# Kernel optimization log

Measured on AMD Instinct MI355X. Metric: run time of the kernel, lower is better.

Reference implementation:

```python
import jax, jax.numpy as jnp
import numpy as np

NUM_GRAPHS = 256
NEG_SLOPE = 0.2


def gat_layer(x, src, dst, W, a_src, a_dst, bias, concat):
    # x: [N, Fin], W: [Fin, H*C], a_src/a_dst: [H, C], bias: [H*C] or [C]
    N = x.shape[0]
    H, C = a_src.shape
    xl = (x @ W).reshape(N, H, C)                      # per-head projections
    e_src = jnp.sum(xl * a_src, axis=-1)               # [N, H]
    e_dst = jnp.sum(xl * a_dst, axis=-1)               # [N, H]
    e = jax.nn.leaky_relu(e_src[src] + e_dst[dst], NEG_SLOPE)  # [E, H]
    # edge softmax over variable-size neighbor sets (grouped by dst)
    m = jax.ops.segment_max(e, dst, num_segments=N)    # [N, H]
    m = jnp.where(jnp.isfinite(m), m, 0.0)
    ee = jnp.exp(e - m[dst])
    s = jax.ops.segment_sum(ee, dst, num_segments=N)   # [N, H]
    alpha = ee / (s[dst] + 1e-16)                      # [E, H]
    msg = alpha[:, :, None] * xl[src]                  # [E, H, C]
    out = jax.ops.segment_sum(msg, dst, num_segments=N)  # [N, H, C]
    out = out.reshape(N, H * C) if concat else out.mean(axis=1)
    return out + bias


def setup_inputs() -> dict:
    key = jax.random.key(0)
    ks = jax.random.split(key, 12)
    N, E, Fin, H, C, Fout = 100000, 1600000, 128, 8, 16, 64
    x = jax.random.normal(ks[0], (N, Fin), dtype=jnp.float32)
    edge_index = jax.random.randint(ks[1], (2, E), 0, N, dtype=jnp.int32)
    batch = jnp.sort(jax.random.randint(ks[2], (N,), 0, NUM_GRAPHS, dtype=jnp.int32))
    sc = 0.1
    W1 = jax.random.normal(ks[3], (Fin, H * C), dtype=jnp.float32) * sc
    att_src1 = jax.random.normal(ks[4], (H, C), dtype=jnp.float32) * sc
    att_dst1 = jax.random.normal(ks[5], (H, C), dtype=jnp.float32) * sc
    bias1 = jnp.zeros((H * C,), dtype=jnp.float32)
    W2 = jax.random.normal(ks[6], (H * C, Fout), dtype=jnp.float32) * sc
    att_src2 = jax.random.normal(ks[7], (1, Fout), dtype=jnp.float32) * sc
    att_dst2 = jax.random.normal(ks[8], (1, Fout), dtype=jnp.float32) * sc
    bias2 = jnp.zeros((Fout,), dtype=jnp.float32)
    return {"x": x, "W1": W1, "att_src1": att_src1, "att_dst1": att_dst1,
            "bias1": bias1, "W2": W2, "att_src2": att_src2, "att_dst2": att_dst2,
            "bias2": bias2, "edge_index": edge_index, "batch": batch}


def reference(x, W1, att_src1, att_dst1, bias1, W2, att_src2, att_dst2, bias2,
              edge_index, batch):
    N = x.shape[0]
    loop = jnp.arange(N, dtype=edge_index.dtype)
    src = jnp.concatenate([edge_index[0], loop])  # add self-loops (PyG default)
    dst = jnp.concatenate([edge_index[1], loop])
    # dropout is identity in eval mode
    h = gat_layer(x, src, dst, W1, att_src1, att_dst1, bias1, concat=True)
    h = jax.nn.elu(h)
    h = gat_layer(h, src, dst, W2, att_src2, att_dst2, bias2, concat=False)
    # global mean pooling over graphs
    sums = jax.ops.segment_sum(h, batch, num_segments=NUM_GRAPHS)
    cnts = jax.ops.segment_sum(jnp.ones((N,), h.dtype), batch, num_segments=NUM_GRAPHS)
    return sums / jnp.maximum(cnts, 1.0)[:, None]
```

## Files before the change

### kernel.cpp

```cpp
#include <hip/hip_runtime.h>
#include <hip/hip_fp16.h>


#define LRELU_SLOPE 0.2f
#define NBLKB 512
#define NBUCK 256

__device__ __forceinline__ float lrelu(float x) { return x > 0.f ? x : LRELU_SLOPE * x; }

typedef _Float16 f16x8 __attribute__((ext_vector_type(8)));
typedef float f32x4 __attribute__((ext_vector_type(4)));

__global__ __launch_bounds__(256) void convWT(const float* __restrict__ W,
    __half* __restrict__ Wt, int K, int M) {
  const int i = blockIdx.x * 256 + threadIdx.x;
  if (i < K * M) {
    const int k = i / M, m = i % M;
    Wt[m * K + k] = __float2half(W[i]);
  }
}

template<typename TX, int M_>
__global__ __launch_bounds__(256) void gemm_mfma(const TX* __restrict__ X,
    const __half* __restrict__ Wt, __half* __restrict__ Y, int N) {
  constexpr int K = 128;
  constexpr int BM = 64;
  constexpr int LP = K + 8;
  __shared__ _Float16 Xl[BM * LP];
  const int tid = threadIdx.x;
  const int row0 = blockIdx.x * BM;

  if constexpr (sizeof(TX) == 4) {
    for (int i = tid; i < BM * (K / 4); i += 256) {
      const int r = i / (K / 4), c4 = (i % (K / 4)) * 4;
      int gr = row0 + r; if (gr >= N) gr = N - 1;
      const float4 v = *(const float4*)((const float*)X + (size_t)gr * K + c4);
      _Float16* d = &Xl[r * LP + c4];
      d[0] = (_Float16)v.x; d[1] = (_Float16)v.y;
      d[2] = (_Float16)v.z; d[3] = (_Float16)v.w;
    }
  } else {
    for (int i = tid; i < BM * (K / 8); i += 256) {
      const int r = i / (K / 8), c8 = (i % (K / 8)) * 8;
      int gr = row0 + r; if (gr >= N) gr = N - 1;
      const f16x8 v = *(const f16x8*)((const _Float16*)X + (size_t)gr * K + c8);
      *(f16x8*)&Xl[r * LP + c8] = v;
    }
  }
  __syncthreads();

  const int w = tid >> 6, l = tid & 63;
  const int lrow = l & 15, lk = (l >> 4) * 8;
  constexpr int NT = M_ / 16;
  f32x4 acc[NT];
#pragma unroll
  for (int n = 0; n < NT; ++n) acc[n] = (f32x4){0.f, 0.f, 0.f, 0.f};

#pragma unroll
  for (int kk = 0; kk < K; kk += 32) {
    const f16x8 a = *(const f16x8*)&Xl[(w * 16 + lrow) * LP + kk + lk];
#pragma unroll
    for (int n = 0; n < NT; ++n) {
      const f16x8 b = *(const f16x8*)((const _Float16*)Wt +
                        (size_t)(n * 16 + lrow) * K + kk + lk);
      acc[n] = __builtin_amdgcn_mfma_f32_16x16x32_f16(a, b, acc[n], 0, 0, 0);
    }
  }
  const int orow = row0 + w * 16 + (l >> 4) * 4;
#pragma unroll
  for (int n = 0; n < NT; ++n) {
#pragma unroll
    for (int j = 0; j < 4; ++j) {
      const int gr = orow + j;
      if (gr < N) Y[(size_t)gr * M_ + n * 16 + lrow] = __float2half(acc[n][j]);
    }
  }
}

__global__ __launch_bounds__(256) void att_h8(const __half* __restrict__ xl,
    const float* __restrict__ as, const float* __restrict__ ad,
    float* __restrict__ es, float* __restrict__ ed, int N) {
  const int n = blockIdx.x * 2 + (threadIdx.x >> 7);
  const int c = threadIdx.x & 127;
  if (n >= N) return;
  const float v = __half2float(xl[(size_t)n * 128 + c]);
  float ps = v * as[c];
  float pd = v * ad[c];
#pragma unroll
  for (int o = 8; o >= 1; o >>= 1) {
    ps += __shfl_xor(ps, o, 16);
    pd += __shfl_xor(pd, o, 16);
  }
  if ((c & 15) == 0) {
    es[n * 8 + (c >> 4)] = ps;
    ed[n * 8 + (c >> 4)] = pd;
  }
}

__global__ __launch_bounds__(256) void att_h1(const __half* __restrict__ xl2,
    const float* __restrict__ as, const float* __restrict__ ad,
    float* __restrict__ es, float* __restrict__ ed, int N) {
  const int n = blockIdx.x * 4 + (threadIdx.x >> 6);
  const int c = threadIdx.x & 63;
  if (n >= N) return;
  const float v = __half2float(xl2[(size_t)n * 64 + c]);
  float ps = v * as[c];
  float pd = v * ad[c];
#pragma unroll
  for (int o = 32; o >= 1; o >>= 1) {
    ps += __shfl_xor(ps, o, 64);
    pd += __shfl_xor(pd, o, 64);
  }
  if (c == 0) { es[n] = ps; ed[n] = pd; }
}

__global__ __launch_bounds__(256) void bucket_hist(const int* __restrict__ ei, int E,
    int* __restrict__ bh) {
  __shared__ int hist[NBUCK];
  const int t = threadIdx.x;
  hist[t] = 0;
  __syncthreads();
  const int chunk = (E + NBLKB - 1) / NBLKB;
  const int s0 = blockIdx.x * chunk;
  const int s1 = min(E, s0 + chunk);
  for (int e = s0 + t; e < s1; e += 256) atomicAdd(&hist[ei[E + e] >> 9], 1);
  __syncthreads();
  bh[t * NBLKB + blockIdx.x] = hist[t];
}

__global__ __launch_bounds__(256) void scanA(int* __restrict__ a, int* __restrict__ ctot, int N) {
  __shared__ int sm[256];
  const int base = blockIdx.x * 1024;
  const int t = threadIdx.x;
  int v[4], s = 0;
#pragma unroll
  for (int i = 0; i < 4; ++i) {
    const int idx = base + t * 4 + i;
    v[i] = (idx < N) ? a[idx] : 0;
    s += v[i];
  }
  sm[t] = s;
  __syncthreads();
  for (int o = 1; o < 256; o <<= 1) {
    const int x = (t >= o) ? sm[t - o] : 0;
    __syncthreads();
    sm[t] += x;
    __syncthreads();
  }
  if (t == 255) ctot[blockIdx.x] = sm[255];
  int run = sm[t] - s;
#pragma unroll
  for (int i = 0; i < 4; ++i) {
    const int idx = base + t * 4 + i;
    if (idx < N) a[idx] = run;
    run += v[i];
  }
}

__global__ __launch_bounds__(128) void scanB(int* __restrict__ ctot, int n) {
  __shared__ int sm[128];
  const int t = threadIdx.x;
  const int v = (t < n) ? ctot[t] : 0;
  sm[t] = v;
  __syncthreads();
  for (int o = 1; o < 128; o <<= 1) {
    const int x = (t >= o) ? sm[t - o] : 0;
    __syncthreads();
    sm[t] += x;
    __syncthreads();
  }
  if (t < n) ctot[t] = sm[t] - v;
}

__global__ __launch_bounds__(256) void scanC(int* __restrict__ a, const int* __restrict__ ctot, int N) {
  const int i = blockIdx.x * 256 + threadIdx.x;
  if (i < N) a[i] += ctot[i >> 10];
}

__global__ __launch_bounds__(256) void bucket_scatter(const int* __restrict__ ei, int E,
    const int* __restrict__ bh, int2* __restrict__ eb) {
  __shared__ int offs[NBUCK];
  const int t = threadIdx.x;
  offs[t] = bh[t * NBLKB + blockIdx.x];
  __syncthreads();
  const int chunk = (E + NBLKB - 1) / NBLKB;
  const int s0 = blockIdx.x * chunk;
  const int s1 = min(E, s0 + chunk);
  for (int e = s0 + t; e < s1; e += 256) {
    const int s = ei[e], d = ei[E + e];
    const int pos = atomicAdd(&offs[d >> 9], 1);
    eb[pos] = make_int2(s, d);
  }
}

__global__ __launch_bounds__(256) void csr_bucket(const int2* __restrict__ eb,
    const int* __restrict__ bh, int E, int N,
    int* __restrict__ rowptr, int* __restrict__ csr) {
  __shared__ int deg[512];
  __shared__ int sm[256];
  const int t = threadIdx.x;
  const int bucket = blockIdx.x;
  const int bstart = bh[bucket * NBLKB];
  const int bend = (bucket + 1 < NBUCK) ? bh[(bucket + 1) * NBLKB] : E;
  const int n0 = bucket << 9;
  deg[t] = 0; deg[t + 256] = 0;
  __syncthreads();
  for (int j = bstart + t; j < bend; j += 256) atomicAdd(&deg[eb[j].y - n0], 1);
  __syncthreads();
  const int v0 = deg[2 * t], v1 = deg[2 * t + 1];
  const int s = v0 + v1;
  sm[t] = s;
  __syncthreads();
  for (int o = 1; o < 256; o <<= 1) {
    const int x = (t >= o) ? sm[t - o] : 0;
    __syncthreads();
    sm[t] += x;
    __syncthreads();
  }
  const int base = sm[t] - s;
  if (n0 + 2 * t < N)     rowptr[n0 + 2 * t]     = bstart + base + v0;
  if (n0 + 2 * t + 1 < N) rowptr[n0 + 2 * t + 1] = bstart + base + v0 + v1;
  deg[2 * t] = base;
  deg[2 * t + 1] = base + v0;
  __syncthreads();
  for (int j = bstart + t; j < bend; j += 256) {
    const int2 e = eb[j];
    const int pos = bstart + atomicAdd(&deg[e.y - n0], 1);
    csr[pos] = e.x;
  }
}

__global__ __launch_bounds__(256) void gather_h8(const __half* __restrict__ xl,
    const float* __restrict__ es, const float* __restrict__ ed,
    const int* __restrict__ rowptr, const int* __restrict__ csr,
    const float* __restrict__ bias, __half* __restrict__ hout, int N) {
  const int wave = threadIdx.x >> 6, lane = threadIdx.x & 63;
  const int n = blockIdx.x * 4 + wave;
  if (n >= N) return;
  const int sub = lane >> 5;
  const int sl  = lane & 31;
  const int c0  = sl * 4;
  const int h   = sl >> 2;
  const float edv = ed[n * 8 + h];
  const int start = (n == 0) ? 0 : rowptr[n - 1];
  const int end   = rowptr[n];
  union U8 { uint2 u; __half2 h2[2]; };

  float4 acc = make_float4(0.f, 0.f, 0.f, 0.f);
  float ssum = 0.f;
  if (sub == 0) {
    const float ee = __expf(lrelu(es[n * 8 + h] + edv));
    U8 r; r.u = *(const uint2*)&xl[(size_t)n * 128 + c0];
    const float2 f0 = __half22float2(r.h2[0]), f1 = __half22float2(r.h2[1]);
    acc.x = ee * f0.x; acc.y = ee * f0.y; acc.z = ee * f1.x; acc.w = ee * f1.y;
    ssum = ee;
  }
  int j = start + sub;
  for (; j + 6 < end; j += 8) {
    int s0 = csr[j], s1 = csr[j + 2], s2 = csr[j + 4], s3 = csr[j + 6];
    float ev[4]; U8 r[4];
    ev[0] = es[s0 * 8 + h]; r[0].u = *(const uint2*)&xl[(size_t)s0 * 128 + c0];
    ev[1] = es[s1 * 8 + h]; r[1].u = *(const uint2*)&xl[(size_t)s1 * 128 + c0];
    ev[2] = es[s2 * 8 + h]; r[2].u = *(const uint2*)&xl[(size_t)s2 * 128 + c0];
    ev[3] = es[s3 * 8 + h]; r[3].u = *(const uint2*)&xl[(size_t)s3 * 128 + c0];
#pragma unroll
    for (int k = 0; k < 4; ++k) {
      const float ee = __expf(lrelu(ev[k] + edv));
      const float2 f0 = __half22float2(r[k].h2[0]), f1 = __half22float2(r[k].h2[1]);
      acc.x += ee * f0.x; acc.y += ee * f0.y;
      acc.z += ee * f1.x; acc.w += ee * f1.y;
      ssum += ee;
    }
  }
  for (; j < end; j += 2) {
    const int src = csr[j];
    const float ee = __expf(lrelu(es[src * 8 + h] + edv));
    U8 r; r.u = *(const uint2*)&xl[(size_t)src * 128 + c0];
    const float2 f0 = __half22float2(r.h2[0]), f1 = __half22float2(r.h2[1]);
    acc.x += ee * f0.x; acc.y += ee * f0.y;
    acc.z += ee * f1.x; acc.w += ee * f1.y;
    ssum += ee;
  }
  acc.x += __shfl_xor(acc.x, 32); acc.y += __shfl_xor(acc.y, 32);
  acc.z += __shfl_xor(acc.z, 32); acc.w += __shfl_xor(acc.w, 32);
  ssum  += __shfl_xor(ssum, 32);
  if (sub == 0) {
    const float inv = 1.f / (ssum + 1e-16f);
    const float4 b4 = *(const float4*)&bias[c0];
    float v0 = acc.x * inv + b4.x, v1 = acc.y * inv + b4.y;
    float v2 = acc.z * inv + b4.z, v3 = acc.w * inv + b4.w;
    v0 = v0 > 0.f ? v0 : __expf(v0) - 1.f;
    v1 = v1 > 0.f ? v1 : __expf(v1) - 1.f;
    v2 = v2 > 0.f ? v2 : __expf(v2) - 1.f;
    v3 = v3 > 0.f ? v3 : __expf(v3) - 1.f;
    U8 o; o.h2[0] = __floats2half2_rn(v0, v1); o.h2[1] = __floats2half2_rn(v2, v3);
    *(uint2*)&hout[(size_t)n * 128 + c0] = o.u;
  }
}

__global__ __launch_bounds__(256) void gather_h1(const __half* __restrict__ xl2,
    const float* __restrict__ es, const float* __restrict__ ed,
    const int* __restrict__ rowptr, const int* __restrict__ csr,
    const float* __restrict__ bias, float* __restrict__ vout, int N) {
  const int wave = threadIdx.x >> 6, lane = threadIdx.x & 63;
  const int n = blockIdx.x * 4 + wave;
  if (n >= N) return;
  const int sub = lane >> 4;
  const int sl  = lane & 15;
  const int c0  = sl * 4;
  const float edv = ed[n];
  const int start = (n == 0) ? 0 : rowptr[n - 1];
  const int end   = rowptr[n];
  union U8 { uint2 u; __half2 h2[2]; };

  float4 acc = make_float4(0.f, 0.f, 0.f, 0.f);
  float ssum = 0.f;
  if (sub == 0) {
    const float ee = __expf(lrelu(es[n] + edv));
    U8 r; r.u = *(const uint2*)&xl2[(size_t)n * 64 + c0];
    const float2 f0 = __half22float2(r.h2[0]), f1 = __half22float2(r.h2[1]);
    acc.x = ee * f0.x; acc.y = ee * f0.y; acc.z = ee * f1.x; acc.w = ee * f1.y;
    ssum = ee;
  }
  int j = start + sub;
  for (; j + 4 < end; j += 8) {
    const int s0 = csr[j], s1 = csr[j + 4];
    const float e0 = es[s0], e1 = es[s1];
    U8 r0, r1;
    r0.u = *(const uint2*)&xl2[(size_t)s0 * 64 + c0];
    r1.u = *(const uint2*)&xl2[(size_t)s1 * 64 + c0];
    {
      const float ee = __expf(lrelu(e0 + edv));
      const float2 f0 = __half22float2(r0.h2[0]), f1 = __half22float2(r0.h2[1]);
      acc.x += ee * f0.x; acc.y += ee * f0.y;
      acc.z += ee * f1.x; acc.w += ee * f1.y; ssum += ee;
    }
    {
      const float ee = __expf(lrelu(e1 + edv));
      const float2 f0 = __half22float2(r1.h2[0]), f1 = __half22float2(r1.h2[1]);
      acc.x += ee * f0.x; acc.y += ee * f0.y;
      acc.z += ee * f1.x; acc.w += ee * f1.y; ssum += ee;
    }
  }
  for (; j < end; j += 4) {
    const int src = csr[j];
    const float ee = __expf(lrelu(es[src] + edv));
    U8 r; r.u = *(const uint2*)&xl2[(size_t)src * 64 + c0];
    const float2 f0 = __half22float2(r.h2[0]), f1 = __half22float2(r.h2[1]);
    acc.x += ee * f0.x; acc.y += ee * f0.y;
    acc.z += ee * f1.x; acc.w += ee * f1.y; ssum += ee;
  }
#pragma unroll
  for (int o = 16; o <= 32; o <<= 1) {
    acc.x += __shfl_xor(acc.x, o); acc.y += __shfl_xor(acc.y, o);
    acc.z += __shfl_xor(acc.z, o); acc.w += __shfl_xor(acc.w, o);
    ssum  += __shfl_xor(ssum, o);
  }
  if (sub == 0) {
    const float inv = 1.f / (ssum + 1e-16f);
    const float4 b4 = *(const float4*)&bias[c0];
    float4 o;
    o.x = acc.x * inv + b4.x; o.y = acc.y * inv + b4.y;
    o.z = acc.z * inv + b4.z; o.w = acc.w * inv + b4.w;
    *(float4*)&vout[(size_t)n * 64 + c0] = o;
  }
}

__global__ __launch_bounds__(256) void pool_seg(const float* __restrict__ v,
    const int* __restrict__ batch, float* __restrict__ out, int N) {
  const int g = blockIdx.x;
  const int t = threadIdx.x;
  int lo = 0, hi = N;
  while (lo < hi) { const int m = (lo + hi) >> 1; if (batch[m] < g) lo = m + 1; else hi = m; }
  const int start = lo;
  hi = N;
  while (lo < hi) { const int m = (lo + hi) >> 1; if (batch[m] <= g) lo = m + 1; else hi = m; }
  const int end = lo;

  const int c = t & 63, rg = t >> 6;
  float s = 0.f;
  for (int r = start + rg; r < end; r += 4) s += v[(size_t)r * 64 + c];
  __shared__ float sm[256];
  sm[t] = s;
  __syncthreads();
  if (t < 64) {
    const float tot = sm[t] + sm[t + 64] + sm[t + 128] + sm[t + 192];
    out[g * 64 + t] = tot / fmaxf((float)(end - start), 1.f);
  }
}

extern "C" void kernel_launch(void* const* d_in, const int* in_sizes, int n_in,
                              void* d_out, int out_size, void* d_ws, size_t ws_size,
                              hipStream_t stream) {
  const float* x   = (const float*)d_in[0];
  const float* W1  = (const float*)d_in[1];
  const float* as1 = (const float*)d_in[2];
  const float* ad1 = (const float*)d_in[3];
  const float* b1  = (const float*)d_in[4];
  const float* W2  = (const float*)d_in[5];
  const float* as2 = (const float*)d_in[6];
  const float* ad2 = (const float*)d_in[7];
  const float* b2  = (const float*)d_in[8];
  const int* ei    = (const int*)d_in[9];
  const int* batch = (const int*)d_in[10];
  float* out = (float*)d_out;
  const int N = in_sizes[10];
  const int E = in_sizes[9] / 2;
  const int G = out_size / 64;
  const int BH = NBUCK * NBLKB;

  char* ws = (char*)d_ws;
  __half* xl  = (__half*)ws;
  __half* h   = (__half*)(ws + (size_t)N * 256);
  __half* xl2 = xl;
  float* vbuf = (float*)(ws + (size_t)N * 256);
  float* es1  = (float*)(ws + (size_t)N * 512);
  float* ed1  = es1 + (size_t)N * 8;
  float* es2  = es1;
  float* ed2  = es1 + N;
  int* rowptr = (int*)(ed1 + (size_t)N * 8);
  int* csr    = rowptr + N;
  int2* eb    = (int2*)((((uintptr_t)(csr + E)) + 7) & ~(uintptr_t)7);
  int* bh     = (int*)(eb + E);
  int* ctot   = bh + BH;
  __half* Wt1 = (__half*)((((uintptr_t)(ctot + 128)) + 31) & ~(uintptr_t)31);
  __half* Wt2 = Wt1 + 128 * 128;

  convWT<<<(128 * 128 + 255) / 256, 256, 0, stream>>>(W1, Wt1, 128, 128);
  convWT<<<(128 * 64 + 255) / 256, 256, 0, stream>>>(W2, Wt2, 128, 64);

  bucket_hist<<<NBLKB, 256, 0, stream>>>(ei, E, bh);
  scanA<<<BH / 1024, 256, 0, stream>>>(bh, ctot, BH);
  scanB<<<1, 128, 0, stream>>>(ctot, BH / 1024);
  scanC<<<BH / 256, 256, 0, stream>>>(bh, ctot, BH);
  bucket_scatter<<<NBLKB, 256, 0, stream>>>(ei, E, bh, eb);
  csr_bucket<<<(N + 511) / 512, 256, 0, stream>>>(eb, bh, E, N, rowptr, csr);

  gemm_mfma<float, 128><<<(N + 63) / 64, 256, 0, stream>>>(x, Wt1, xl, N);
  att_h8<<<(N + 1) / 2, 256, 0, stream>>>(xl, as1, ad1, es1, ed1, N);
  gather_h8<<<(N + 3) / 4, 256, 0, stream>>>(xl, es1, ed1, rowptr, csr, b1, h, N);

  gemm_mfma<__half, 64><<<(N + 63) / 64, 256, 0, stream>>>(h, Wt2, xl2, N);
  att_h1<<<(N + 3) / 4, 256, 0, stream>>>(xl2, as2, ad2, es2, ed2, N);
  gather_h1<<<(N + 3) / 4, 256, 0, stream>>>(xl2, es2, ed2, rowptr, csr, b2, vbuf, N);

  pool_seg<<<G, 256, 0, stream>>>(vbuf, batch, out, N);
}
```

Measured before the change: 321.2 us.

## Fuse attention scores into GEMM epilogue, pack edge buffer, widen CSR build blocks

The per-node attention dot products move into the MFMA GEMM epilogue using lane shuffles, which removes the att_h8 and att_h1 kernels and their re-reads of xl. The two weight-transpose launches merge into one kernel. The edge bucket buffer packs src and local dst into one int instead of int2, halving its traffic. The hist, scatter and CSR kernels use larger blocks (1024/512 threads), with one deg slot per thread in csr_bucket. Packing assumes src < 2^22, which holds for N=100000, and es/ed are now computed from fp32 accumulators rather than the fp16-rounded outputs.

```diff
diff --git a/kernel.cpp b/kernel.cpp
--- a/kernel.cpp
+++ b/kernel.cpp
@@ -11,18 +11,26 @@
 typedef _Float16 f16x8 __attribute__((ext_vector_type(8)));
 typedef float f32x4 __attribute__((ext_vector_type(4)));
 
-__global__ __launch_bounds__(256) void convWT(const float* __restrict__ W,
-    __half* __restrict__ Wt, int K, int M) {
+__global__ __launch_bounds__(256) void convWT2(const float* __restrict__ W1,
+    const float* __restrict__ W2, __half* __restrict__ Wt1, __half* __restrict__ Wt2) {
   const int i = blockIdx.x * 256 + threadIdx.x;
-  if (i < K * M) {
-    const int k = i / M, m = i % M;
-    Wt[m * K + k] = __float2half(W[i]);
-  }
-}
-
-template<typename TX, int M_>
+  if (i < 128 * 128) {
+    const int k = i >> 7, m = i & 127;
+    Wt1[m * 128 + k] = __float2half(W1[i]);
+  } else {
+    const int j = i - 128 * 128;
+    if (j < 128 * 64) {
+      const int k = j >> 6, m = j & 63;
+      Wt2[m * 128 + k] = __float2half(W2[j]);
+    }
+  }
+}
+
+template<typename TX, int M_, int HEADS>
 __global__ __launch_bounds__(256) void gemm_mfma(const TX* __restrict__ X,
-    const __half* __restrict__ Wt, __half* __restrict__ Y, int N) {
+    const __half* __restrict__ Wt, __half* __restrict__ Y,
+    const float* __restrict__ as, const float* __restrict__ ad,
+    float* __restrict__ es, float* __restrict__ ed, int N) {
   constexpr int K = 128;
   constexpr int BM = 64;
   constexpr int LP = K + 8;
@@ -75,57 +83,59 @@
       if (gr < N) Y[(size_t)gr * M_ + n * 16 + lrow] = __float2half(acc[n][j]);
     }
   }
-}
-
-__global__ __launch_bounds__(256) void att_h8(const __half* __restrict__ xl,
-    const float* __restrict__ as, const float* __restrict__ ad,
-    float* __restrict__ es, float* __restrict__ ed, int N) {
-  const int n = blockIdx.x * 2 + (threadIdx.x >> 7);
-  const int c = threadIdx.x & 127;
-  if (n >= N) return;
-  const float v = __half2float(xl[(size_t)n * 128 + c]);
-  float ps = v * as[c];
-  float pd = v * ad[c];
-#pragma unroll
-  for (int o = 8; o >= 1; o >>= 1) {
-    ps += __shfl_xor(ps, o, 16);
-    pd += __shfl_xor(pd, o, 16);
-  }
-  if ((c & 15) == 0) {
-    es[n * 8 + (c >> 4)] = ps;
-    ed[n * 8 + (c >> 4)] = pd;
-  }
-}
-
-__global__ __launch_bounds__(256) void att_h1(const __half* __restrict__ xl2,
-    const float* __restrict__ as, const float* __restrict__ ad,
-    float* __restrict__ es, float* __restrict__ ed, int N) {
-  const int n = blockIdx.x * 4 + (threadIdx.x >> 6);
-  const int c = threadIdx.x & 63;
-  if (n >= N) return;
-  const float v = __half2float(xl2[(size_t)n * 64 + c]);
-  float ps = v * as[c];
-  float pd = v * ad[c];
-#pragma unroll
-  for (int o = 32; o >= 1; o >>= 1) {
-    ps += __shfl_xor(ps, o, 64);
-    pd += __shfl_xor(pd, o, 64);
-  }
-  if (c == 0) { es[n] = ps; ed[n] = pd; }
-}
-
-__global__ __launch_bounds__(256) void bucket_hist(const int* __restrict__ ei, int E,
+
+  if constexpr (HEADS == 8) {
+#pragma unroll
+    for (int n = 0; n < NT; ++n) {
+#pragma unroll
+      for (int j = 0; j < 4; ++j) {
+        float ps = acc[n][j] * as[n * 16 + lrow];
+        float pd = acc[n][j] * ad[n * 16 + lrow];
+#pragma unroll
+        for (int o = 1; o <= 8; o <<= 1) {
+          ps += __shfl_xor(ps, o);
+          pd += __shfl_xor(pd, o);
+        }
+        if (lrow == n) {
+          const int gr = orow + j;
+          if (gr < N) { es[gr * 8 + n] = ps; ed[gr * 8 + n] = pd; }
+        }
+      }
+    }
+  } else {
+#pragma unroll
+    for (int j = 0; j < 4; ++j) {
+      float ps = 0.f, pd = 0.f;
+#pragma unroll
+      for (int n = 0; n < NT; ++n) {
+        ps += acc[n][j] * as[n * 16 + lrow];
+        pd += acc[n][j] * ad[n * 16 + lrow];
+      }
+#pragma unroll
+      for (int o = 1; o <= 8; o <<= 1) {
+        ps += __shfl_xor(ps, o);
+        pd += __shfl_xor(pd, o);
+      }
+      if (lrow == 0) {
+        const int gr = orow + j;
+        if (gr < N) { es[gr] = ps; ed[gr] = pd; }
+      }
+    }
+  }
+}
+
+__global__ __launch_bounds__(1024) void bucket_hist(const int* __restrict__ ei, int E,
     int* __restrict__ bh) {
   __shared__ int hist[NBUCK];
   const int t = threadIdx.x;
-  hist[t] = 0;
+  if (t < NBUCK) hist[t] = 0;
   __syncthreads();
   const int chunk = (E + NBLKB - 1) / NBLKB;
   const int s0 = blockIdx.x * chunk;
   const int s1 = min(E, s0 + chunk);
-  for (int e = s0 + t; e < s1; e += 256) atomicAdd(&hist[ei[E + e] >> 9], 1);
-  __syncthreads();
-  bh[t * NBLKB + blockIdx.x] = hist[t];
+  for (int e = s0 + t; e < s1; e += 1024) atomicAdd(&hist[ei[E + e] >> 9], 1);
+  __syncthreads();
+  if (t < NBUCK) bh[t * NBLKB + blockIdx.x] = hist[t];
 }
 
 __global__ __launch_bounds__(256) void scanA(int* __restrict__ a, int* __restrict__ ctot, int N) {
@@ -177,56 +187,52 @@
   if (i < N) a[i] += ctot[i >> 10];
 }
 
-__global__ __launch_bounds__(256) void bucket_scatter(const int* __restrict__ ei, int E,
-    const int* __restrict__ bh, int2* __restrict__ eb) {
+__global__ __launch_bounds__(1024) void bucket_scatter(const int* __restrict__ ei, int E,
+    const int* __restrict__ bh, int* __restrict__ eb) {
   __shared__ int offs[NBUCK];
   const int t = threadIdx.x;
-  offs[t] = bh[t * NBLKB + blockIdx.x];
+  if (t < NBUCK) offs[t] = bh[t * NBLKB + blockIdx.x];
   __syncthreads();
   const int chunk = (E + NBLKB - 1) / NBLKB;
   const int s0 = blockIdx.x * chunk;
   const int s1 = min(E, s0 + chunk);
-  for (int e = s0 + t; e < s1; e += 256) {
+  for (int e = s0 + t; e < s1; e += 1024) {
     const int s = ei[e], d = ei[E + e];
     const int pos = atomicAdd(&offs[d >> 9], 1);
-    eb[pos] = make_int2(s, d);
-  }
-}
-
-__global__ __launch_bounds__(256) void csr_bucket(const int2* __restrict__ eb,
+    eb[pos] = (s << 9) | (d & 511);
+  }
+}
+
+__global__ __launch_bounds__(512) void csr_bucket(const int* __restrict__ eb,
     const int* __restrict__ bh, int E, int N,
     int* __restrict__ rowptr, int* __restrict__ csr) {
   __shared__ int deg[512];
-  __shared__ int sm[256];
+  __shared__ int sm[512];
   const int t = threadIdx.x;
   const int bucket = blockIdx.x;
   const int bstart = bh[bucket * NBLKB];
   const int bend = (bucket + 1 < NBUCK) ? bh[(bucket + 1) * NBLKB] : E;
   const int n0 = bucket << 9;
-  deg[t] = 0; deg[t + 256] = 0;
-  __syncthreads();
-  for (int j = bstart + t; j < bend; j += 256) atomicAdd(&deg[eb[j].y - n0], 1);
-  __syncthreads();
-  const int v0 = deg[2 * t], v1 = deg[2 * t + 1];
-  const int s = v0 + v1;
-  sm[t] = s;
-  __syncthreads();
-  for (int o = 1; o < 256; o <<= 1) {
+  deg[t] = 0;
+  __syncthreads();
+  for (int j = bstart + t; j < bend; j += 512) atomicAdd(&deg[eb[j] & 511], 1);
+  __syncthreads();
+  const int v = deg[t];
+  sm[t] = v;
+  __syncthreads();
+  for (int o = 1; o < 512; o <<= 1) {
     const int x = (t >= o) ? sm[t - o] : 0;
     __syncthreads();
     sm[t] += x;
     __syncthreads();
   }
-  const int base = sm[t] - s;
-  if (n0 + 2 * t < N)     rowptr[n0 + 2 * t]     = bstart + base + v0;
-  if (n0 + 2 * t + 1 < N) rowptr[n0 + 2 * t + 1] = bstart + base + v0 + v1;
-  deg[2 * t] = base;
-  deg[2 * t + 1] = base + v0;
-  __syncthreads();
-  for (int j = bstart + t; j < bend; j += 256) {
-    const int2 e = eb[j];
-    const int pos = bstart + atomicAdd(&deg[e.y - n0], 1);
-    csr[pos] = e.x;
+  if (n0 + t < N) rowptr[n0 + t] = bstart + sm[t];
+  deg[t] = bstart + sm[t] - v;
+  __syncthreads();
+  for (int j = bstart + t; j < bend; j += 512) {
+    const int e = eb[j];
+    const int pos = atomicAdd(&deg[e & 511], 1);
+    csr[pos] = e >> 9;
   }
 }
 
@@ -420,28 +426,25 @@
   float* ed2  = es1 + N;
   int* rowptr = (int*)(ed1 + (size_t)N * 8);
   int* csr    = rowptr + N;
-  int2* eb    = (int2*)((((uintptr_t)(csr + E)) + 7) & ~(uintptr_t)7);
-  int* bh     = (int*)(eb + E);
+  int* eb     = csr + E;
+  int* bh     = eb + E;
   int* ctot   = bh + BH;
   __half* Wt1 = (__half*)((((uintptr_t)(ctot + 128)) + 31) & ~(uintptr_t)31);
   __half* Wt2 = Wt1 + 128 * 128;
 
-  convWT<<<(128 * 128 + 255) / 256, 256, 0, stream>>>(W1, Wt1, 128, 128);
-  convWT<<<(128 * 64 + 255) / 256, 256, 0, stream>>>(W2, Wt2, 128, 64);
-
-  bucket_hist<<<NBLKB, 256, 0, stream>>>(ei, E, bh);
+  convWT2<<<(128 * 128 + 128 * 64 + 255) / 256, 256, 0, stream>>>(W1, W2, Wt1, Wt2);
+
+  bucket_hist<<<NBLKB, 1024, 0, stream>>>(ei, E, bh);
   scanA<<<BH / 1024, 256, 0, stream>>>(bh, ctot, BH);
   scanB<<<1, 128, 0, stream>>>(ctot, BH / 1024);
   scanC<<<BH / 256, 256, 0, stream>>>(bh, ctot, BH);
-  bucket_scatter<<<NBLKB, 256, 0, stream>>>(ei, E, bh, eb);
-  csr_bucket<<<(N + 511) / 512, 256, 0, stream>>>(eb, bh, E, N, rowptr, csr);
-
-  gemm_mfma<float, 128><<<(N + 63) / 64, 256, 0, stream>>>(x, Wt1, xl, N);
-  att_h8<<<(N + 1) / 2, 256, 0, stream>>>(xl, as1, ad1, es1, ed1, N);
+  bucket_scatter<<<NBLKB, 1024, 0, stream>>>(ei, E, bh, eb);
+  csr_bucket<<<(N + 511) / 512, 512, 0, stream>>>(eb, bh, E, N, rowptr, csr);
+
+  gemm_mfma<float, 128, 8><<<(N + 63) / 64, 256, 0, stream>>>(x, Wt1, xl, as1, ad1, es1, ed1, N);
   gather_h8<<<(N + 3) / 4, 256, 0, stream>>>(xl, es1, ed1, rowptr, csr, b1, h, N);
 
-  gemm_mfma<__half, 64><<<(N + 63) / 64, 256, 0, stream>>>(h, Wt2, xl2, N);
-  att_h1<<<(N + 3) / 4, 256, 0, stream>>>(xl2, as2, ad2, es2, ed2, N);
+  gemm_mfma<__half, 64, 1><<<(N + 63) / 64, 256, 0, stream>>>(h, Wt2, xl2, as2, ad2, es2, ed2, N);
   gather_h1<<<(N + 3) / 4, 256, 0, stream>>>(xl2, es2, ed2, rowptr, csr, b2, vbuf, N);
 
   pool_seg<<<G, 256, 0, stream>>>(vbuf, batch, out, N);
```

Result: faster. 286.9 us (-10.7%).
